# Kernel tuning notes

Measured on AMD Instinct MI355X. Metric: run time of the kernel, lower is better.

The kernel has to match this reference:

```python
import jax, jax.numpy as jnp
import numpy as np

B, S, DIM = 2, 2048, 2048
NH, NKV = 32, 8
HD = DIM // NH  # 64


def setup_inputs() -> dict:
    key = jax.random.key(0)
    ks = jax.random.split(key, 6)
    x = jax.random.normal(ks[0], (B, S, DIM), jnp.float32)
    # realistic rotary tables: [S, HD//2]
    inv_freq = 1.0 / (10000.0 ** (jnp.arange(0, HD, 2, dtype=jnp.float32) / HD))
    freqs = jnp.arange(S, dtype=jnp.float32)[:, None] * inv_freq[None, :]
    cos, sin = jnp.cos(freqs), jnp.sin(freqs)
    init = lambda k, shape: jax.random.normal(k, shape, jnp.float32) * (shape[0] ** -0.5)
    Wq = init(ks[1], (DIM, NH * HD))
    Wk = init(ks[2], (DIM, NKV * HD))
    Wv = init(ks[3], (DIM, NKV * HD))
    Wo = init(ks[4], (NH * HD, DIM))
    return {"x": x, "cos": cos, "sin": sin, "Wq": Wq, "Wk": Wk, "Wv": Wv, "Wo": Wo}


def _rope(t, c, s):
    # t: [B, S, H, HD]; c, s: [1, S, 1, HD//2]; consecutive-pair (v1) style
    b, sl, h, hd = t.shape
    tp = t.reshape(b, sl, h, hd // 2, 2)
    t0, t1 = tp[..., 0], tp[..., 1]
    return jnp.stack([t0 * c - t1 * s, t0 * s + t1 * c], axis=-1).reshape(b, sl, h, hd)


def reference(x, cos, sin, Wq, Wk, Wv, Wo):
    b, sl, _ = x.shape
    q = (x @ Wq).reshape(b, sl, NH, HD)
    k = (x @ Wk).reshape(b, sl, NKV, HD)
    v = (x @ Wv).reshape(b, sl, NKV, HD)
    c = cos[None, :, None, :]
    s = sin[None, :, None, :]
    q = _rope(q, c, s)
    k = _rope(k, c, s)
    n_rep = NH // NKV
    k = jnp.repeat(k, n_rep, axis=2)  # GQA repeat_interleave over heads
    v = jnp.repeat(v, n_rep, axis=2)
    scale = 1.0 / np.sqrt(HD)
    scores = jnp.einsum("bqhd,bkhd->bhqk", q, k) * scale  # [B, H, S, S]
    causal = jnp.tril(jnp.ones((sl, sl), dtype=bool))
    scores = jnp.where(causal[None, None], scores, -jnp.inf)
    p = jax.nn.softmax(scores, axis=-1)
    out = jnp.einsum("bhqk,bkhd->bqhd", p, v).reshape(b, sl, NH * HD)
    return out @ Wo
```

## Files before the change

kernel.cpp:

```cpp
#include <hip/hip_runtime.h>
#include <hip/hip_bf16.h>


typedef __attribute__((ext_vector_type(8))) short short8;
typedef __attribute__((ext_vector_type(4))) float f32x4;
typedef __attribute__((ext_vector_type(16))) float f32x16;
typedef __attribute__((ext_vector_type(2))) int i32x2;
typedef __attribute__((ext_vector_type(4))) int i32x4;

__device__ __forceinline__ unsigned short f2bfu(float f){
  unsigned u = __float_as_uint(f);
  u += 0x7FFFu + ((u >> 16) & 1u);
  return (unsigned short)(u >> 16);
}
__device__ __forceinline__ float bfu2f(unsigned short u){
  return __uint_as_float(((unsigned)u) << 16);
}
__device__ __forceinline__ unsigned cvt_pk_bf16(float lo, float hi){
  unsigned r;
  asm("v_cvt_pk_bf16_f32 %0, %1, %2" : "=v"(r) : "v"(lo), "v"(hi));
  return r;
}
__device__ __forceinline__ i32x2 pl32swap(int a, int b){
  auto r = __builtin_amdgcn_permlane32_swap(a, b, false, false);
  return __builtin_bit_cast(i32x2, r);
}
__device__ __forceinline__ int swz64(int row, int slot){
  return row * 64 + (((slot) ^ (row & 7)) << 3);
}
template<int N> __device__ __forceinline__ void vm_wait(){
  if constexpr (N == 8)      asm volatile("s_waitcnt vmcnt(8)" ::: "memory");
  else if constexpr (N == 7) asm volatile("s_waitcnt vmcnt(7)" ::: "memory");
  else if constexpr (N == 6) asm volatile("s_waitcnt vmcnt(6)" ::: "memory");
  else if constexpr (N == 4) asm volatile("s_waitcnt vmcnt(4)" ::: "memory");
  else if constexpr (N == 3) asm volatile("s_waitcnt vmcnt(3)" ::: "memory");
  else if constexpr (N == 2) asm volatile("s_waitcnt vmcnt(2)" ::: "memory");
  else                       asm volatile("s_waitcnt vmcnt(0)" ::: "memory");
}

__global__ void convx_kernel(const float* __restrict__ x, unsigned short* __restrict__ xb, int n4){
  int i = blockIdx.x * blockDim.x + threadIdx.x;
  if (i >= n4) return;
  float4 v = reinterpret_cast<const float4*>(x)[i];
  ushort4 o;
  o.x = f2bfu(v.x); o.y = f2bfu(v.y); o.z = f2bfu(v.z); o.w = f2bfu(v.w);
  reinterpret_cast<ushort4*>(xb)[i] = o;
}

__global__ void transpose_conv_kernel(const float* __restrict__ in, unsigned short* __restrict__ out,
                                      int Min, int Nin){
  __shared__ float t[32][33];
  int c0 = blockIdx.x * 32, r0 = blockIdx.y * 32;
  int tx = threadIdx.x, ty = threadIdx.y;
  #pragma unroll
  for (int i = ty; i < 32; i += 8) t[i][tx] = in[(size_t)(r0 + i) * Nin + c0 + tx];
  __syncthreads();
  #pragma unroll
  for (int i = ty; i < 32; i += 8) out[(size_t)(c0 + i) * Min + r0 + tx] = f2bfu(t[tx][i]);
}

#define PH(SLOT,KK,QM,WAITER,STG) { \
  const unsigned short* sAc = &sA[SLOT][(KK)*8192]; \
  const unsigned short* sBc = &sB[SLOT][(KK)*RB]; \
  short8 afr[4]; \
  afr[0] = *reinterpret_cast<const short8*>(sAc + aOff[(QM)*4+0]); \
  afr[1] = *reinterpret_cast<const short8*>(sAc + aOff[(QM)*4+1]); \
  afr[2] = *reinterpret_cast<const short8*>(sAc + aOff[(QM)*4+2]); \
  afr[3] = *reinterpret_cast<const short8*>(sAc + aOff[(QM)*4+3]); \
  if ((QM) == 0){ \
    _Pragma("unroll") for (int n_ = 0; n_ < NF; n_++) \
      bfr[n_] = *reinterpret_cast<const short8*>(sBc + bOff[n_]); \
  } \
  STG; \
  __builtin_amdgcn_s_barrier(); \
  asm volatile("s_waitcnt lgkmcnt(0)" ::: "memory"); \
  __builtin_amdgcn_sched_barrier(0); \
  __builtin_amdgcn_s_setprio(1); \
  _Pragma("unroll") for (int i_ = 0; i_ < 4; i_++){ \
    _Pragma("unroll") for (int n_ = 0; n_ < NF; n_++){ \
      acc[(QM)*4+i_][n_] = __builtin_amdgcn_mfma_f32_16x16x32_bf16(afr[i_], bfr[n_], acc[(QM)*4+i_][n_], 0, 0, 0); }} \
  __builtin_amdgcn_s_setprio(0); \
  WAITER; \
  __builtin_amdgcn_s_barrier(); \
}

template<int NF, bool OUTBF16>
__global__ __launch_bounds__(512, 2) void gemm8p_kernel(const unsigned short* __restrict__ A,
                                                        const unsigned short* __restrict__ B,
                                                        void* __restrict__ Cp,
                                                        int M, int N, int K, int nbx){
  constexpr int RB  = NF * 2048;
  constexpr int VMS = (NF == 4) ? 8 : (NF == 3 ? 7 : 6);
  __shared__ unsigned short sA[2][16384];
  __shared__ unsigned short sB[2][2 * RB];
  const int tid = threadIdx.x;
  const int l = tid & 63, w = tid >> 6;
  const int quad = l >> 4, c16 = l & 15;
  const int cpx = (int)gridDim.x >> 3;
  const int id2 = ((int)blockIdx.x & 7) * cpx + ((int)blockIdx.x >> 3);
  const int bx = id2 % nbx, by = id2 / nbx;
  const int row0 = by * 256, col0 = bx * (NF * 64);
  const int wr = w >> 2, wc = w & 3;

  const int rlA0 = w * 32 + (l >> 2), rlA1 = rlA0 + 16;
  const unsigned short* gA0 = A + (size_t)(row0 + rlA0) * K + (((l & 3) ^ ((rlA0 >> 1) & 3)) << 3);
  const unsigned short* gA1 = A + (size_t)(row0 + rlA1) * K + (((l & 3) ^ ((rlA1 >> 1) & 3)) << 3);
  const unsigned short* gB0;
  const unsigned short* gB1 = nullptr;
  const unsigned short* gB2 = nullptr;
  if constexpr (NF == 4){
    gB0 = B + (size_t)(col0 + rlA0) * K + (((l & 3) ^ ((rlA0 >> 1) & 3)) << 3);
    gB1 = B + (size_t)(col0 + rlA1) * K + (((l & 3) ^ ((rlA1 >> 1) & 3)) << 3);
  } else {
    const int rlB0 = w * 16 + (l >> 2);
    gB0 = B + (size_t)(col0 + rlB0) * K + (((l & 3) ^ ((rlB0 >> 1) & 3)) << 3);
    if constexpr (NF == 3){
      const int rlB2 = 128 + (w & 3) * 16 + (l >> 2);
      gB2 = B + (size_t)(col0 + rlB2) * K + (((l & 3) ^ ((rlB2 >> 1) & 3)) << 3);
    }
  }

  auto stA = [&](int slot, int kk, int col){
    __builtin_amdgcn_global_load_lds((const __attribute__((address_space(1))) void*)(gA0 + col),
        (__attribute__((address_space(3))) void*)(&sA[slot][kk * 8192 + w * 1024]), 16, 0, 0);
    __builtin_amdgcn_global_load_lds((const __attribute__((address_space(1))) void*)(gA1 + col),
        (__attribute__((address_space(3))) void*)(&sA[slot][kk * 8192 + w * 1024 + 512]), 16, 0, 0);
  };
  auto stB = [&](int slot, int kk, int col){
    if constexpr (NF == 4){
      __builtin_amdgcn_global_load_lds((const __attribute__((address_space(1))) void*)(gB0 + col),
          (__attribute__((address_space(3))) void*)(&sB[slot][kk * RB + w * 1024]), 16, 0, 0);
      __builtin_amdgcn_global_load_lds((const __attribute__((address_space(1))) void*)(gB1 + col),
          (__attribute__((address_space(3))) void*)(&sB[slot][kk * RB + w * 1024 + 512]), 16, 0, 0);
    } else if constexpr (NF == 3){
      __builtin_amdgcn_global_load_lds((const __attribute__((address_space(1))) void*)(gB0 + col),
          (__attribute__((address_space(3))) void*)(&sB[slot][kk * RB + w * 512]), 16, 0, 0);
      if ((kk == 0) ? (w < 4) : (w >= 4))
        __builtin_amdgcn_global_load_lds((const __attribute__((address_space(1))) void*)(gB2 + col),
            (__attribute__((address_space(3))) void*)(&sB[slot][kk * RB + 4096 + (w & 3) * 512]), 16, 0, 0);
    } else {
      __builtin_amdgcn_global_load_lds((const __attribute__((address_space(1))) void*)(gB0 + col),
          (__attribute__((address_space(3))) void*)(&sB[slot][kk * RB + w * 512]), 16, 0, 0);
    }
  };

  int aOff[8], bOff[4];
  #pragma unroll
  for (int mf = 0; mf < 8; mf++){
    int row = wr * 128 + mf * 16 + c16;
    aOff[mf] = row * 32 + ((quad ^ ((row >> 1) & 3)) << 3);
  }
  #pragma unroll
  for (int nf = 0; nf < 4; nf++){
    int row = wc * (NF * 16) + nf * 16 + c16;
    bOff[nf] = row * 32 + ((quad ^ ((row >> 1) & 3)) << 3);
  }

  stA(0, 0, 0);  stB(0, 0, 0);
  stA(0, 1, 32); stB(0, 1, 32);
  stA(1, 0, 64); stB(1, 0, 64);
  vm_wait<VMS>();
  __builtin_amdgcn_s_barrier();

  f32x4 acc[8][4] = {};
  short8 bfr[4];
  const int NI = K >> 7;
  #pragma unroll 1
  for (int j = 0; j < NI - 1; ++j){
    const int t1c  = (2 * j + 1) * 64 + 32;
    const int t2c0 = (2 * j + 2) * 64;
    const int t2c1 = t2c0 + 32;
    const int t3c0 = (2 * j + 3) * 64;
    PH(0,0,0, (void)0,        stA(1,1,t1c))
    PH(0,0,1, vm_wait<VMS>(), stB(1,1,t1c))
    PH(0,1,0, (void)0,        stA(0,0,t2c0))
    PH(0,1,1, vm_wait<VMS>(), stB(0,0,t2c0))
    PH(1,0,0, (void)0,        stA(0,1,t2c1))
    PH(1,0,1, vm_wait<VMS>(), stB(0,1,t2c1))
    PH(1,1,0, (void)0,        stA(1,0,t3c0))
    PH(1,1,1, vm_wait<VMS>(), stB(1,0,t3c0))
  }
  {
    const int t1c = K - 32;
    PH(0,0,0, (void)0,        stA(1,1,t1c))
    PH(0,0,1, vm_wait<VMS>(), stB(1,1,t1c))
    PH(0,1,0, (void)0, ;)
    PH(0,1,1, vm_wait<3>(), ;)
    PH(1,0,0, (void)0, ;)
    PH(1,0,1, vm_wait<0>(), ;)
    PH(1,1,0, (void)0, ;)
    PH(1,1,1, (void)0, ;)
  }

  #pragma unroll
  for (int mf = 0; mf < 8; mf++)
    #pragma unroll
    for (int nf = 0; nf < NF; nf++)
      #pragma unroll
      for (int r = 0; r < 4; r++){
        size_t off = (size_t)(row0 + wr * 128 + mf * 16 + quad * 4 + r) * N + (col0 + wc * (NF * 16) + nf * 16 + c16);
        if (OUTBF16) ((unsigned short*)Cp)[off] = f2bfu(acc[mf][nf][r]);
        else         ((float*)Cp)[off] = acc[mf][nf][r];
      }
}

__global__ void rope_kernel(const unsigned short* __restrict__ qkv, const float* __restrict__ cosb,
                            const float* __restrict__ sinb, unsigned short* __restrict__ Qo,
                            unsigned short* __restrict__ Ko){
  int idx = blockIdx.x * 256 + threadIdx.x;
  const int NQ = 4096 * 1024;
  if (idx < NQ){
    int m = idx >> 10, p = idx & 1023;
    int h = p >> 5, i = p & 31;
    int s = m & 2047;
    unsigned pr = *reinterpret_cast<const unsigned*>(qkv + (size_t)m * 3072 + h * 64 + 2 * i);
    float t0 = bfu2f((unsigned short)(pr & 0xFFFFu));
    float t1 = bfu2f((unsigned short)(pr >> 16));
    float c = cosb[s * 32 + i], sn = sinb[s * 32 + i];
    const float SC = 0.18033688011112042f;
    float o0 = (t0 * c - t1 * sn) * SC;
    float o1 = (t0 * sn + t1 * c) * SC;
    unsigned ow = (unsigned)f2bfu(o0) | ((unsigned)f2bfu(o1) << 16);
    *reinterpret_cast<unsigned*>(Qo + (size_t)m * 2048 + h * 64 + 2 * i) = ow;
  } else {
    int j = idx - NQ;
    int m = j >> 8, p = j & 255;
    int kvh = p >> 5, i = p & 31;
    int s = m & 2047, b = m >> 11;
    unsigned pr = *reinterpret_cast<const unsigned*>(qkv + (size_t)m * 3072 + 2048 + kvh * 64 + 2 * i);
    float t0 = bfu2f((unsigned short)(pr & 0xFFFFu));
    float t1 = bfu2f((unsigned short)(pr >> 16));
    float c = cosb[s * 32 + i], sn = sinb[s * 32 + i];
    float o0 = t0 * c - t1 * sn;
    float o1 = t0 * sn + t1 * c;
    unsigned ow = (unsigned)f2bfu(o0) | ((unsigned)f2bfu(o1) << 16);
    *reinterpret_cast<unsigned*>(Ko + ((size_t)(b * 8 + kvh) * 2048 + s) * 64 + 2 * i) = ow;
  }
}

__global__ void vtrans_kernel(const unsigned short* __restrict__ qkv, unsigned short* __restrict__ Vt){
  __shared__ float t[64][65];
  int bh = blockIdx.y;
  int s0 = blockIdx.x * 64;
  int b = bh >> 3, kvh = bh & 7;
  int tid = threadIdx.x;
  #pragma unroll
  for (int it = 0; it < 16; it++){
    int id = it * 256 + tid;
    int sl = id >> 6, d = id & 63;
    unsigned short u = qkv[(size_t)(b * 2048 + s0 + sl) * 3072 + 2560 + kvh * 64 + d];
    t[sl][d] = bfu2f(u);
  }
  __syncthreads();
  #pragma unroll
  for (int it = 0; it < 16; it++){
    int id = it * 256 + tid;
    int dl = id >> 6, sl = id & 63;
    Vt[((size_t)(b * 8 + kvh) * 64 + dl) * 2048 + s0 + sl] = f2bfu(t[sl][dl]);
  }
}

__global__ __launch_bounds__(256) void attn_kernel(const unsigned short* __restrict__ Q,
                                                   const unsigned short* __restrict__ Kt,
                                                   const unsigned short* __restrict__ Vt,
                                                   unsigned short* __restrict__ O){
  __shared__ unsigned short sK[2][64 * 64];
  __shared__ unsigned short sV[2][64 * 64];
  const int tid = threadIdx.x;
  const int l = tid & 63, w = tid >> 6;
  const int q32 = l & 31, hi = l >> 5;
  const int bid = blockIdx.x;
  const int qt = 15 - (bid >> 6);
  const int bh = bid & 63;
  const int b = bh >> 5, h = bh & 31, kvh = h >> 2;
  const int q0w = qt * 128 + w * 32;
  const int nt = 2 * qt + 2;

  const unsigned short* Kb = Kt + (size_t)(b * 8 + kvh) * 2048 * 64;
  const unsigned short* Vb = Vt + (size_t)(b * 8 + kvh) * 64 * 2048;

  auto stage = [&](int kv0, int buf){
    #pragma unroll
    for (int c = 0; c < 2; c++){
      const int rl = w * 16 + c * 8 + (l >> 3);
      const int ce = (((l & 7) ^ (l >> 3)) << 3);
      __builtin_amdgcn_global_load_lds(
        (const __attribute__((address_space(1))) void*)(Kb + (size_t)(kv0 + rl) * 64 + ce),
        (__attribute__((address_space(3))) void*)(&sK[buf][(w * 16 + c * 8) * 64]), 16, 0, 0);
      __builtin_amdgcn_global_load_lds(
        (const __attribute__((address_space(1))) void*)(Vb + (size_t)rl * 2048 + kv0 + ce),
        (__attribute__((address_space(3))) void*)(&sV[buf][(w * 16 + c * 8) * 64]), 16, 0, 0);
    }
  };

  short8 qv[4];
  {
    const unsigned short* Qp = Q + (size_t)(b * 2048 + q0w + q32) * 2048 + h * 64 + hi * 8;
    #pragma unroll
    for (int kd = 0; kd < 4; kd++) qv[kd] = *reinterpret_cast<const short8*>(Qp + kd * 16);
  }

  const short8 ones = {0x3F80, 0x3F80, 0x3F80, 0x3F80, 0x3F80, 0x3F80, 0x3F80, 0x3F80};

  f32x16 accA = {}, accB = {};
  f32x16 accl = {};
  float m_run = -1e30f;

#define MKAP(Z, R0, AP) { \
    unsigned A_ = cvt_pk_bf16(Z[R0+0], Z[R0+1]); \
    unsigned B_ = cvt_pk_bf16(Z[R0+2], Z[R0+3]); \
    unsigned C_ = cvt_pk_bf16(Z[R0+4], Z[R0+5]); \
    unsigned D_ = cvt_pk_bf16(Z[R0+6], Z[R0+7]); \
    i32x2 s1_ = pl32swap((int)A_, (int)C_); \
    i32x2 s2_ = pl32swap((int)B_, (int)D_); \
    i32x4 q_ = {s1_[0], s2_[0], s1_[1], s2_[1]}; \
    AP = __builtin_bit_cast(short8, q_); \
  }

  stage(0, 0);
  vm_wait<0>();
  __builtin_amdgcn_s_barrier();

  for (int t = 0; t < nt; ++t){
    const int kv0 = t * 64;
    const int buf = t & 1;
    if (t + 1 < nt) stage((t + 1) * 64, buf ^ 1);

    const unsigned short* sKc = &sK[buf][0];
    const unsigned short* sVc = &sV[buf][0];

    f32x16 z0 = {}, z1 = {};
    __builtin_amdgcn_s_setprio(1);
    #pragma unroll
    for (int kd = 0; kd < 4; kd++){
      const int u = kd * 2 + hi;
      short8 ak0 = *reinterpret_cast<const short8*>(&sKc[swz64(q32, u)]);
      short8 ak1 = *reinterpret_cast<const short8*>(&sKc[swz64(32 + q32, u)]);
      z0 = __builtin_amdgcn_mfma_f32_32x32x16_bf16(ak0, qv[kd], z0, 0, 0, 0);
      z1 = __builtin_amdgcn_mfma_f32_32x32x16_bf16(ak1, qv[kd], z1, 0, 0, 0);
    }
    __builtin_amdgcn_s_setprio(0);

    if (kv0 + 63 > q0w){
      const int qg = q0w + q32;
      #pragma unroll
      for (int r = 0; r < 16; r++){
        const int kr = (r & 3) + 8 * (r >> 2) + 4 * hi;
        if (kv0 + kr > qg)      z0[r] = -1e30f;
        if (kv0 + 32 + kr > qg) z1[r] = -1e30f;
      }
    }

    float tm = fmaxf(z0[0], z0[1]);
    #pragma unroll
    for (int r = 2; r < 16; r++) tm = fmaxf(tm, z0[r]);
    #pragma unroll
    for (int r = 0; r < 16; r++) tm = fmaxf(tm, z1[r]);
    tm = fmaxf(tm, __shfl_xor(tm, 32));

    if (!__all(tm <= m_run + 8.0f)){
      float mn = fmaxf(m_run, tm);
      float al = __builtin_amdgcn_exp2f(m_run - mn);
      m_run = mn;
      #pragma unroll
      for (int r = 0; r < 16; r++){
        const int qrow = (r & 3) + 8 * (r >> 2) + 4 * hi;
        float alr = __shfl(al, qrow);
        accA[r] *= alr; accB[r] *= alr; accl[r] *= alr;
      }
    }

    #pragma unroll
    for (int r = 0; r < 16; r++){
      z0[r] = __builtin_amdgcn_exp2f(z0[r] - m_run);
      z1[r] = __builtin_amdgcn_exp2f(z1[r] - m_run);
    }

    short8 apA, apB;
    __builtin_amdgcn_s_setprio(1);
    MKAP(z0, 0, apA)
    MKAP(z0, 8, apB)
    accl = __builtin_amdgcn_mfma_f32_32x32x16_bf16(apA, ones, accl, 0, 0, 0);
    accl = __builtin_amdgcn_mfma_f32_32x32x16_bf16(apB, ones, accl, 0, 0, 0);
    {
      short8 bv;
      bv = *reinterpret_cast<const short8*>(&sVc[swz64(q32, 0 * 2 + hi)]);
      accA = __builtin_amdgcn_mfma_f32_32x32x16_bf16(apA, bv, accA, 0, 0, 0);
      bv = *reinterpret_cast<const short8*>(&sVc[swz64(q32, 1 * 2 + hi)]);
      accA = __builtin_amdgcn_mfma_f32_32x32x16_bf16(apB, bv, accA, 0, 0, 0);
      bv = *reinterpret_cast<const short8*>(&sVc[swz64(32 + q32, 0 * 2 + hi)]);
      accB = __builtin_amdgcn_mfma_f32_32x32x16_bf16(apA, bv, accB, 0, 0, 0);
      bv = *reinterpret_cast<const short8*>(&sVc[swz64(32 + q32, 1 * 2 + hi)]);
      accB = __builtin_amdgcn_mfma_f32_32x32x16_bf16(apB, bv, accB, 0, 0, 0);
    }
    MKAP(z1, 0, apA)
    MKAP(z1, 8, apB)
    accl = __builtin_amdgcn_mfma_f32_32x32x16_bf16(apA, ones, accl, 0, 0, 0);
    accl = __builtin_amdgcn_mfma_f32_32x32x16_bf16(apB, ones, accl, 0, 0, 0);
    {
      short8 bv;
      bv = *reinterpret_cast<const short8*>(&sVc[swz64(q32, 2 * 2 + hi)]);
      accA = __builtin_amdgcn_mfma_f32_32x32x16_bf16(apA, bv, accA, 0, 0, 0);
      bv = *reinterpret_cast<const short8*>(&sVc[swz64(q32, 3 * 2 + hi)]);
      accA = __builtin_amdgcn_mfma_f32_32x32x16_bf16(apB, bv, accA, 0, 0, 0);
      bv = *reinterpret_cast<const short8*>(&sVc[swz64(32 + q32, 2 * 2 + hi)]);
      accB = __builtin_amdgcn_mfma_f32_32x32x16_bf16(apA, bv, accB, 0, 0, 0);
      bv = *reinterpret_cast<const short8*>(&sVc[swz64(32 + q32, 3 * 2 + hi)]);
      accB = __builtin_amdgcn_mfma_f32_32x32x16_bf16(apB, bv, accB, 0, 0, 0);
    }
    __builtin_amdgcn_s_setprio(0);

    vm_wait<0>();
    __builtin_amdgcn_s_barrier();
  }
#undef MKAP

  #pragma unroll
  for (int r = 0; r < 16; r++){
    const float inv = 1.0f / accl[r];
    const int qrow = q0w + (r & 3) + 8 * (r >> 2) + 4 * hi;
    const size_t base = (size_t)(b * 2048 + qrow) * 2048 + h * 64 + q32;
    O[base]      = f2bfu(accA[r] * inv);
    O[base + 32] = f2bfu(accB[r] * inv);
  }
}

extern "C" void kernel_launch(void* const* d_in, const int* in_sizes, int n_in,
                              void* d_out, int out_size, void* d_ws, size_t ws_size,
                              hipStream_t stream){
  (void)in_sizes; (void)n_in; (void)out_size; (void)ws_size;
  const float* x  = (const float*)d_in[0];
  const float* cb = (const float*)d_in[1];
  const float* sb = (const float*)d_in[2];
  const float* Wq = (const float*)d_in[3];
  const float* Wk = (const float*)d_in[4];
  const float* Wv = (const float*)d_in[5];
  const float* Wo = (const float*)d_in[6];
  float* out = (float*)d_out;
  char* ws = (char*)d_ws;

  unsigned short* qkv = (unsigned short*)(ws + 0);
  unsigned short* xb  = (unsigned short*)(ws + 25165824);
  unsigned short* wt  = (unsigned short*)(ws + 41943040);
  unsigned short* qb  = (unsigned short*)(ws + 54525952);
  unsigned short* kb  = (unsigned short*)(ws + 71303168);
  unsigned short* vt  = (unsigned short*)(ws + 75497472);

  dim3 tb(32, 8);
  convx_kernel<<<8192, 256, 0, stream>>>(x, xb, 2097152);
  transpose_conv_kernel<<<dim3(64, 64), tb, 0, stream>>>(Wq, wt, 2048, 2048);
  transpose_conv_kernel<<<dim3(16, 64), tb, 0, stream>>>(Wk, wt + (size_t)2048 * 2048, 2048, 512);
  transpose_conv_kernel<<<dim3(16, 64), tb, 0, stream>>>(Wv, wt + (size_t)2560 * 2048, 2048, 512);
  gemm8p_kernel<3, true><<<256, 512, 0, stream>>>(xb, wt, qkv, 4096, 3072, 2048, 16);
  rope_kernel<<<20480, 256, 0, stream>>>(qkv, cb, sb, qb, kb);
  vtrans_kernel<<<dim3(32, 16), 256, 0, stream>>>(qkv, vt);
  transpose_conv_kernel<<<dim3(64, 64), tb, 0, stream>>>(Wo, wt, 2048, 2048);
  attn_kernel<<<1024, 256, 0, stream>>>(qb, kb, vt, xb);
  gemm8p_kernel<2, false><<<256, 512, 0, stream>>>(xb, wt, out, 4096, 2048, 2048, 16);
}
```

Before: 210.9 us.

## Fuse RoPE, Q scaling and V transpose into QKV GEMM epilogue

The QKV projection GEMM now applies rotary embedding and Q scaling in its epilogue, exchanging pair values with a lane shuffle. It writes Q, K (head-major) and transposed V straight to their final buffers. This removes the separate rope and V-transpose kernels and the round trip through the intermediate qkv buffer. In exchange the epilogue does scattered 2-byte stores, strided ones for V^T, and reads cos/sin per element, which may make the GEMM tail slower.

```diff
diff --git a/kernel.cpp b/kernel.cpp
--- a/kernel.cpp
+++ b/kernel.cpp
@@ -84,11 +84,16 @@
   __builtin_amdgcn_s_barrier(); \
 }
 
-template<int NF, bool OUTBF16>
+template<int NF, int MODE>
 __global__ __launch_bounds__(512, 2) void gemm8p_kernel(const unsigned short* __restrict__ A,
                                                         const unsigned short* __restrict__ B,
                                                         void* __restrict__ Cp,
-                                                        int M, int N, int K, int nbx){
+                                                        int M, int N, int K, int nbx,
+                                                        const float* __restrict__ cosb,
+                                                        const float* __restrict__ sinb,
+                                                        unsigned short* __restrict__ qb,
+                                                        unsigned short* __restrict__ kbp,
+                                                        unsigned short* __restrict__ vtp){
   constexpr int RB  = NF * 2048;
   constexpr int VMS = (NF == 4) ? 8 : (NF == 3 ? 7 : 6);
   __shared__ unsigned short sA[2][16384];
@@ -192,71 +197,49 @@
     PH(1,1,1, (void)0, ;)
   }
 
-  #pragma unroll
-  for (int mf = 0; mf < 8; mf++)
-    #pragma unroll
-    for (int nf = 0; nf < NF; nf++)
+  if constexpr (MODE == 0){
+    #pragma unroll
+    for (int mf = 0; mf < 8; mf++)
       #pragma unroll
-      for (int r = 0; r < 4; r++){
-        size_t off = (size_t)(row0 + wr * 128 + mf * 16 + quad * 4 + r) * N + (col0 + wc * (NF * 16) + nf * 16 + c16);
-        if (OUTBF16) ((unsigned short*)Cp)[off] = f2bfu(acc[mf][nf][r]);
-        else         ((float*)Cp)[off] = acc[mf][nf][r];
+      for (int nf = 0; nf < NF; nf++)
+        #pragma unroll
+        for (int r = 0; r < 4; r++){
+          size_t off = (size_t)(row0 + wr * 128 + mf * 16 + quad * 4 + r) * N + (col0 + wc * (NF * 16) + nf * 16 + c16);
+          ((float*)Cp)[off] = acc[mf][nf][r];
+        }
+  } else {
+    const float SCq = 0.18033688011112042f;
+    #pragma unroll
+    for (int mf = 0; mf < 8; mf++){
+      #pragma unroll
+      for (int nf = 0; nf < NF; nf++){
+        const int ocol = col0 + wc * (NF * 16) + nf * 16 + c16;
+        const int d = ocol & 63;
+        const int i = d >> 1, p = ocol & 1;
+        #pragma unroll
+        for (int r = 0; r < 4; r++){
+          const int orow = row0 + wr * 128 + mf * 16 + quad * 4 + r;
+          const int s = orow & 2047, bb = orow >> 11;
+          float v0 = acc[mf][nf][r];
+          if (ocol < 2560){
+            float pv = __shfl_xor(v0, 1);
+            float cc = cosb[s * 32 + i], sn = sinb[s * 32 + i];
+            float t0 = p ? pv : v0;
+            float t1 = p ? v0 : pv;
+            float o = p ? (t0 * sn + t1 * cc) : (t0 * cc - t1 * sn);
+            if (ocol < 2048){
+              qb[(size_t)orow * 2048 + ocol] = f2bfu(o * SCq);
+            } else {
+              const int kvh = (ocol - 2048) >> 6;
+              kbp[((size_t)(bb * 8 + kvh) * 2048 + s) * 64 + d] = f2bfu(o);
+            }
+          } else {
+            const int kvh = (ocol - 2560) >> 6;
+            vtp[((size_t)(bb * 8 + kvh) * 64 + d) * 2048 + s] = f2bfu(v0);
+          }
+        }
       }
-}
-
-__global__ void rope_kernel(const unsigned short* __restrict__ qkv, const float* __restrict__ cosb,
-                            const float* __restrict__ sinb, unsigned short* __restrict__ Qo,
-                            unsigned short* __restrict__ Ko){
-  int idx = blockIdx.x * 256 + threadIdx.x;
-  const int NQ = 4096 * 1024;
-  if (idx < NQ){
-    int m = idx >> 10, p = idx & 1023;
-    int h = p >> 5, i = p & 31;
-    int s = m & 2047;
-    unsigned pr = *reinterpret_cast<const unsigned*>(qkv + (size_t)m * 3072 + h * 64 + 2 * i);
-    float t0 = bfu2f((unsigned short)(pr & 0xFFFFu));
-    float t1 = bfu2f((unsigned short)(pr >> 16));
-    float c = cosb[s * 32 + i], sn = sinb[s * 32 + i];
-    const float SC = 0.18033688011112042f;
-    float o0 = (t0 * c - t1 * sn) * SC;
-    float o1 = (t0 * sn + t1 * c) * SC;
-    unsigned ow = (unsigned)f2bfu(o0) | ((unsigned)f2bfu(o1) << 16);
-    *reinterpret_cast<unsigned*>(Qo + (size_t)m * 2048 + h * 64 + 2 * i) = ow;
-  } else {
-    int j = idx - NQ;
-    int m = j >> 8, p = j & 255;
-    int kvh = p >> 5, i = p & 31;
-    int s = m & 2047, b = m >> 11;
-    unsigned pr = *reinterpret_cast<const unsigned*>(qkv + (size_t)m * 3072 + 2048 + kvh * 64 + 2 * i);
-    float t0 = bfu2f((unsigned short)(pr & 0xFFFFu));
-    float t1 = bfu2f((unsigned short)(pr >> 16));
-    float c = cosb[s * 32 + i], sn = sinb[s * 32 + i];
-    float o0 = t0 * c - t1 * sn;
-    float o1 = t0 * sn + t1 * c;
-    unsigned ow = (unsigned)f2bfu(o0) | ((unsigned)f2bfu(o1) << 16);
-    *reinterpret_cast<unsigned*>(Ko + ((size_t)(b * 8 + kvh) * 2048 + s) * 64 + 2 * i) = ow;
-  }
-}
-
-__global__ void vtrans_kernel(const unsigned short* __restrict__ qkv, unsigned short* __restrict__ Vt){
-  __shared__ float t[64][65];
-  int bh = blockIdx.y;
-  int s0 = blockIdx.x * 64;
-  int b = bh >> 3, kvh = bh & 7;
-  int tid = threadIdx.x;
-  #pragma unroll
-  for (int it = 0; it < 16; it++){
-    int id = it * 256 + tid;
-    int sl = id >> 6, d = id & 63;
-    unsigned short u = qkv[(size_t)(b * 2048 + s0 + sl) * 3072 + 2560 + kvh * 64 + d];
-    t[sl][d] = bfu2f(u);
-  }
-  __syncthreads();
-  #pragma unroll
-  for (int it = 0; it < 16; it++){
-    int id = it * 256 + tid;
-    int dl = id >> 6, sl = id & 63;
-    Vt[((size_t)(b * 8 + kvh) * 64 + dl) * 2048 + s0 + sl] = f2bfu(t[sl][dl]);
+    }
   }
 }
 
@@ -439,7 +422,6 @@
   float* out = (float*)d_out;
   char* ws = (char*)d_ws;
 
-  unsigned short* qkv = (unsigned short*)(ws + 0);
   unsigned short* xb  = (unsigned short*)(ws + 25165824);
   unsigned short* wt  = (unsigned short*)(ws + 41943040);
   unsigned short* qb  = (unsigned short*)(ws + 54525952);
@@ -451,10 +433,10 @@
   transpose_conv_kernel<<<dim3(64, 64), tb, 0, stream>>>(Wq, wt, 2048, 2048);
   transpose_conv_kernel<<<dim3(16, 64), tb, 0, stream>>>(Wk, wt + (size_t)2048 * 2048, 2048, 512);
   transpose_conv_kernel<<<dim3(16, 64), tb, 0, stream>>>(Wv, wt + (size_t)2560 * 2048, 2048, 512);
-  gemm8p_kernel<3, true><<<256, 512, 0, stream>>>(xb, wt, qkv, 4096, 3072, 2048, 16);
-  rope_kernel<<<20480, 256, 0, stream>>>(qkv, cb, sb, qb, kb);
-  vtrans_kernel<<<dim3(32, 16), 256, 0, stream>>>(qkv, vt);
+  gemm8p_kernel<3, 2><<<256, 512, 0, stream>>>(xb, wt, nullptr, 4096, 3072, 2048, 16,
+                                               cb, sb, qb, kb, vt);
   transpose_conv_kernel<<<dim3(64, 64), tb, 0, stream>>>(Wo, wt, 2048, 2048);
   attn_kernel<<<1024, 256, 0, stream>>>(qb, kb, vt, xb);
-  gemm8p_kernel<2, false><<<256, 512, 0, stream>>>(xb, wt, out, 4096, 2048, 2048, 16);
-}
+  gemm8p_kernel<2, 0><<<256, 512, 0, stream>>>(xb, wt, out, 4096, 2048, 2048, 16,
+                                               nullptr, nullptr, nullptr, nullptr, nullptr);
+}
```

Result: slower. 222.0 us (+5.3%).
